# Optimization experiments

Hardware: AMD Instinct MI355X
Metric: run time of the kernel (lower is better)

The kernel has to match this reference:

```python
import jax, jax.numpy as jnp
import numpy as np


def setup_inputs() -> dict:
    key = jax.random.key(0)
    B, E, K = 1024, 1024, 64
    k0, k1, k2, k3, k4, k5 = jax.random.split(key, 6)
    s = 1.0 / np.sqrt(E)  # PyTorch GRU init bound
    c = jax.random.normal(k0, (B, E), dtype=jnp.float32)
    x = jax.random.normal(k1, (B, E, K), dtype=jnp.float32)
    W_ih = jax.random.uniform(k2, (3 * E, E), minval=-s, maxval=s, dtype=jnp.float32)
    W_hh = jax.random.uniform(k3, (3 * E, E), minval=-s, maxval=s, dtype=jnp.float32)
    b_ih = jax.random.uniform(k4, (3 * E,), minval=-s, maxval=s, dtype=jnp.float32)
    b_hh = jax.random.uniform(k5, (3 * E,), minval=-s, maxval=s, dtype=jnp.float32)
    return {"c": c, "x": x, "W_ih": W_ih, "W_hh": W_hh, "b_ih": b_ih, "b_hh": b_hh, "K": K}


def reference(c, x, W_ih, W_hh, b_ih, b_hh, K):
    # c: (B, E) initial hidden state; x: (B, E, T) teacher-forcing sequence.
    # Inputs actually consumed by the GRU: zeros at step 0, then x columns
    # [T-K .. T-2] at steps 1..K-1 (the torch slice at the last step is empty
    # and never used).
    B, E = c.shape
    T = x.shape[2]
    x_t = jnp.transpose(x, (2, 0, 1))  # (T, B, E)
    xs = jnp.concatenate(
        [jnp.zeros((1, B, E), dtype=x.dtype), x_t[T - K : T - 1]], axis=0
    )  # (K, B, E)

    def step(h, xk):
        gi = xk @ W_ih.T + b_ih  # (B, 3E)
        gh = h @ W_hh.T + b_hh   # (B, 3E)
        i_r, i_z, i_n = jnp.split(gi, 3, axis=-1)
        h_r, h_z, h_n = jnp.split(gh, 3, axis=-1)
        r = jax.nn.sigmoid(i_r + h_r)
        z = jax.nn.sigmoid(i_z + h_z)
        n = jnp.tanh(i_n + r * h_n)
        h_new = (1.0 - z) * n + z * h
        return h_new, h_new

    _, ys = jax.lax.scan(step, c, xs)  # ys: (K, B, E)
    y = jnp.transpose(ys, (1, 0, 2))   # (B, K, E) == torch.cat(y_out, dim=1)
    return jnp.transpose(y, (0, 2, 1))  # teacher-forcing transpose -> (B, E, K)
```

## Files before the change

### kernel.cpp

```cpp
#include <hip/hip_runtime.h>
#include <hip/hip_bf16.h>
#include <math.h>

typedef __bf16 bf16x8 __attribute__((ext_vector_type(8)));
typedef float f32x4 __attribute__((ext_vector_type(4)));
typedef unsigned short u16x8 __attribute__((ext_vector_type(8)));

__device__ inline unsigned short f2b(float f) {
  union { float f; unsigned u; } v; v.f = f;
  unsigned u = v.u;
  return (unsigned short)((u + 0x7fffu + ((u >> 16) & 1u)) >> 16);
}
__device__ inline float b2f(unsigned short s) {
  union { unsigned u; float f; } v; v.u = ((unsigned)s) << 16;
  return v.f;
}
__device__ inline float sigm(float x) { return 1.f / (1.f + __expf(-x)); }
__device__ inline float tanh_f(float x) {
  float e = __expf(2.f * x);
  return 1.f - 2.f / (e + 1.f);
}
__device__ inline void gll16(const unsigned short* g, unsigned short* l) {
  __builtin_amdgcn_global_load_lds(
      (const __attribute__((address_space(1))) void*)g,
      (__attribute__((address_space(3))) void*)l, 16, 0, 0);
}
__device__ inline void gll16u(const unsigned short* g, unsigned short* l) {
  __builtin_amdgcn_global_load_lds(
      (const __attribute__((address_space(1))) void*)g,
      (__attribute__((address_space(3))) void*)l, 16, 0, 17);
}
__device__ inline void as64(unsigned short* p, unsigned long long v) {
  __hip_atomic_store((unsigned long long*)p, v, __ATOMIC_RELAXED,
                     __HIP_MEMORY_SCOPE_AGENT);
}

__global__ __launch_bounds__(256) void prep_kernel(
    const float* __restrict__ Wih, const float* __restrict__ Whh,
    const float* __restrict__ c, unsigned short* __restrict__ Wihb,
    unsigned short* __restrict__ Whhb, unsigned short* __restrict__ hbf,
    float* __restrict__ h32, long nW, long nH)
{
  long stride = (long)gridDim.x * blockDim.x;
  long t0 = (long)blockIdx.x * blockDim.x + threadIdx.x;
  for (long i = t0; i < nW; i += stride) {
    Wihb[i] = f2b(Wih[i]);
    Whhb[i] = f2b(Whh[i]);
  }
  for (long i = t0; i < nH; i += stride) {
    float v = c[i];
    h32[i] = v;
    hbf[i] = f2b(v);
  }
}

__global__ __launch_bounds__(256) void reorder_kernel(
    const unsigned short* __restrict__ Wihb, const unsigned short* __restrict__ Whhb,
    const float* __restrict__ bih, const float* __restrict__ bhh,
    unsigned short* __restrict__ Wihp, unsigned short* __restrict__ Whhp,
    float* __restrict__ bihp, float* __restrict__ bhhp, int E)
{
  int N3 = 3 * E;
  long total = (long)N3 * E;
  long stride = (long)gridDim.x * blockDim.x;
  long t0 = (long)blockIdx.x * blockDim.x + threadIdx.x;
  for (long i = t0; i < total; i += stride) {
    int rp = (int)(i / E);
    int col = (int)(i - (long)rp * E);
    int g6 = rp / 192, rem = rp - g6 * 192;
    int g = rem >> 6, elo = rem & 63;
    long src = ((long)g * E + g6 * 64 + elo) * E + col;
    Wihp[i] = Wihb[src];
    Whhp[i] = Whhb[src];
  }
  for (long i = t0; i < N3; i += stride) {
    int rp = (int)i;
    int g6 = rp / 192, rem = rp - g6 * 192;
    int g = rem >> 6, elo = rem & 63;
    bihp[i] = bih[(long)g * E + g6 * 64 + elo];
    bhhp[i] = bhh[(long)g * E + g6 * 64 + elo];
  }
}

__global__ __launch_bounds__(256) void transpose_x(
    const float* __restrict__ x, unsigned short* __restrict__ XS,
    int B, int E, int K)
{
  __shared__ float T[64][65];
  int e0 = blockIdx.x * 64;
  int b = blockIdx.y;
  int t = threadIdx.x;
  const float* xb = x + ((long)b * E + e0) * K;
#pragma unroll
  for (int i = 0; i < 4; ++i) {
    int cidx = i * 256 + t;
    int e = cidx >> 4;
    int f4 = cidx & 15;
    float4 v = *(const float4*)(xb + (long)e * K + f4 * 4);
    T[e][f4 * 4 + 0] = v.x;
    T[e][f4 * 4 + 1] = v.y;
    T[e][f4 * 4 + 2] = v.z;
    T[e][f4 * 4 + 3] = v.w;
  }
  __syncthreads();
#pragma unroll
  for (int i = 0; i < 16; ++i) {
    int cidx = i * 256 + t;
    int k = cidx >> 6;
    int e = cidx & 63;
    if (k < K - 1)
      XS[((long)(k + 1) * B + b) * E + e0 + e] = f2b(T[e][k]);
  }
}

#define BM 128
#define BN 128
#define BKS 64

template<int OUTBF>
__global__ __launch_bounds__(256)
void gemm_bt(const unsigned short* __restrict__ A,
             const unsigned short* __restrict__ Bw,
             const float* __restrict__ bias,
             float* __restrict__ Cf, unsigned short* __restrict__ Cb,
             int M, int N, int K)
{
  __shared__ __align__(16) unsigned short As[BM * BKS];
  __shared__ __align__(16) unsigned short Bs[BN * BKS];

  int nwg = gridDim.x * gridDim.y;
  int wg = blockIdx.y * gridDim.x + blockIdx.x;
  if ((nwg & 7) == 0) { int ch = nwg >> 3; wg = (wg & 7) * ch + (wg >> 3); }
  int tx = wg % gridDim.x;
  int ty = wg / gridDim.x;

  const int tid = threadIdx.x;
  const int lane = tid & 63;
  const int wave = tid >> 6;
  const int wr = wave >> 1, wc = wave & 1;

  f32x4 acc[4][4] = {};

  const long a_base = (long)ty * BM * K;
  const long b_base = (long)tx * BN * K;

  for (int kt = 0; kt < K; kt += BKS) {
    __syncthreads();
#pragma unroll
    for (int i = 0; i < 4; ++i) {
      int c = i * 256 + tid;
      int row = c >> 3, sc = c & 7;
      int gcol8 = sc ^ (row & 7);
      const unsigned short* ga = A + a_base + (long)row * K + kt + gcol8 * 8;
      const unsigned short* gb = Bw + b_base + (long)row * K + kt + gcol8 * 8;
      int cbase = (i * 256 + wave * 64) * 8;
      gll16(ga, &As[cbase]);
      gll16(gb, &Bs[cbase]);
    }
    __syncthreads();
#pragma unroll
    for (int kk = 0; kk < BKS; kk += 32) {
      int kidx = kk + ((lane >> 4) << 3);
      int c8 = kidx >> 3;
      bf16x8 af[4], bfv[4];
#pragma unroll
      for (int m = 0; m < 4; ++m) {
        int row = wr * 64 + m * 16 + (lane & 15);
        af[m] = *(const bf16x8*)&As[row * BKS + ((c8 ^ (row & 7)) << 3)];
      }
#pragma unroll
      for (int n = 0; n < 4; ++n) {
        int col = wc * 64 + n * 16 + (lane & 15);
        bfv[n] = *(const bf16x8*)&Bs[col * BKS + ((c8 ^ (col & 7)) << 3)];
      }
#pragma unroll
      for (int m = 0; m < 4; ++m)
#pragma unroll
        for (int n = 0; n < 4; ++n)
          acc[m][n] = __builtin_amdgcn_mfma_f32_16x16x32_bf16(
              af[m], bfv[n], acc[m][n], 0, 0, 0);
    }
  }

  long crow0 = (long)ty * BM + wr * 64;
  long ccol0 = (long)tx * BN + wc * 64;
#pragma unroll
  for (int m = 0; m < 4; ++m) {
#pragma unroll
    for (int n = 0; n < 4; ++n) {
      long col = ccol0 + n * 16 + (lane & 15);
      float bv = bias[col];
#pragma unroll
      for (int j = 0; j < 4; ++j) {
        long row = crow0 + m * 16 + ((lane >> 4) << 2) + j;
        float v = acc[m][n][j] + bv;
        if (OUTBF) Cb[row * N + col] = f2b(v);
        else       Cf[row * N + col] = v;
      }
    }
  }
}

#define VMW(N) asm volatile("s_waitcnt vmcnt(" #N ")" ::: "memory")

__global__ __launch_bounds__(512, 1)
void gru_rec4(const unsigned short* __restrict__ GI,
              const unsigned short* __restrict__ Whp,
              const float* __restrict__ bhp,
              const unsigned short* __restrict__ h0,
              unsigned short* __restrict__ hbuf0,
              unsigned short* __restrict__ hbuf1,
              unsigned short* __restrict__ Y,
              unsigned int* __restrict__ bar,
              int B, int E, int K, int net)
{
  __shared__ __align__(16) unsigned char smem[156672];
  unsigned short* Ah  = (unsigned short*)smem;
  unsigned short* Bss = (unsigned short*)(smem + 49152);
  unsigned short* GIs = (unsigned short*)(smem + 122880);
  unsigned short* Ys  = (unsigned short*)(smem + 147456);
  float* Red = (float*)smem;

  const int N3 = 3 * E;
  const int e6 = blockIdx.x;
  const int bt = blockIdx.y;
  const int b0 = bt << 6;
  const int ec0 = e6 * 192;
  const int ecol0 = e6 << 6;
  const int tid = threadIdx.x;
  const int lane = tid & 63;
  const int w = tid >> 6;
  const int ew = w >> 1;
  const int kw = w & 1;
  const int q = lane >> 4;
  const int l15 = lane & 15;
  const int el = (ew << 4) + l15;
  const int c8 = (kw << 2) + q;
  const int axo = (c8 ^ (l15 & 7)) << 3;
  const int bxo = (c8 ^ (el & 7)) << 3;

  const int arow = tid >> 3;
  const int ag8 = (tid & 7) ^ (arow & 7);
  const long a_goff = (long)(b0 + arow) * E + ag8 * 8;
  const int a_dst = tid * 8;
  long b_goff[3]; int b_dst[3];
#pragma unroll
  for (int i = 0; i < 3; ++i) {
    int c = i * 512 + tid;
    int row = c >> 3;
    int g8 = (c & 7) ^ (row & 7);
    b_goff[i] = (long)(ec0 + row) * E + g8 * 8;
    b_dst[i] = c * 8;
  }
  long gi_off[3]; int gi_dst[3];
#pragma unroll
  for (int i = 0; i < 3; ++i) {
    int c = i * 512 + tid;
    int row = c / 24, cc = c - row * 24;
    gi_off[i] = (long)(b0 + row) * N3 + ec0 + cc * 8;
    gi_dst[i] = c * 8;
  }

  const float bh0 = bhp[ec0 + el];
  const float bh1 = bhp[ec0 + 64 + el];
  const float bh2 = bhp[ec0 + 128 + el];

  if (kw == 0) {
#pragma unroll
    for (int m = 0; m < 4; ++m)
#pragma unroll
      for (int j = 0; j < 4; ++j) {
        int row = m * 16 + q * 4 + j;
        Ys[row * 72 + el] = h0[(long)(b0 + row) * E + ecol0 + el];
      }
  }
  __syncthreads();

  for (int k = 0; k < K; ++k) {
    const unsigned short* hprev = (k & 1) ? hbuf1 : hbuf0;
    unsigned short* hnext = (k & 1) ? hbuf0 : hbuf1;
    const unsigned short* GIk = GI + (long)k * B * N3;

#pragma unroll
    for (int i = 0; i < 3; ++i) gll16(GIk + gi_off[i], GIs + gi_dst[i]);
#pragma unroll
    for (int t = 0; t < 5; ++t)
      gll16u(hprev + a_goff + t * 64, Ah + t * 4096 + a_dst);
#pragma unroll
    for (int t = 0; t < 2; ++t)
#pragma unroll
      for (int i = 0; i < 3; ++i)
        gll16(Whp + b_goff[i] + t * 64, Bss + t * 12288 + b_dst[i]);

    f32x4 acc[4][3];
#pragma unroll
    for (int m = 0; m < 4; ++m)
#pragma unroll
      for (int g = 0; g < 3; ++g)
        acc[m][g] = (f32x4){0.f, 0.f, 0.f, 0.f};

#pragma unroll
    for (int kt = 0; kt < 16; ++kt) {
      if (kt == 0)       VMW(3);
      else if (kt == 1)  VMW(4);
      else if (kt <= 11) VMW(5);
      else if (kt == 12) VMW(4);
      else if (kt == 15) VMW(0);
      else               VMW(3);
      asm volatile("s_waitcnt lgkmcnt(0)" ::: "memory");
      __builtin_amdgcn_s_barrier();
      asm volatile("" ::: "memory");

      if (kt + 2 < 16) {
#pragma unroll
        for (int i = 0; i < 3; ++i)
          gll16(Whp + b_goff[i] + (kt + 2) * 64,
                Bss + ((kt + 2) % 3) * 12288 + b_dst[i]);
      }
      if (kt + 5 < 16)
        gll16u(hprev + a_goff + (kt + 5) * 64,
               Ah + ((kt + 5) % 6) * 4096 + a_dst);

      const unsigned short* Ab = Ah + (kt % 6) * 4096;
      const unsigned short* Bb = Bss + (kt % 3) * 12288;
      bf16x8 af[4], bfg[3];
#pragma unroll
      for (int m = 0; m < 4; ++m)
        af[m] = *(const bf16x8*)&Ab[(m * 16 + l15) * 64 + axo];
#pragma unroll
      for (int g = 0; g < 3; ++g)
        bfg[g] = *(const bf16x8*)&Bb[(g * 64 + el) * 64 + bxo];

      __builtin_amdgcn_s_setprio(1);
#pragma unroll
      for (int g = 0; g < 3; ++g)
#pragma unroll
        for (int m = 0; m < 4; ++m)
          acc[m][g] = __builtin_amdgcn_mfma_f32_16x16x32_bf16(
              af[m], bfg[g], acc[m][g], 0, 0, 0);
      __builtin_amdgcn_s_setprio(0);
    }

    __syncthreads();
    float* rp = &Red[((ew << 6) + lane) * 49];
    if (kw == 1) {
#pragma unroll
      for (int m = 0; m < 4; ++m)
#pragma unroll
        for (int g = 0; g < 3; ++g)
#pragma unroll
          for (int cc = 0; cc < 4; ++cc)
            rp[(m * 3 + g) * 4 + cc] = acc[m][g][cc];
    }
    __syncthreads();
    if (kw == 0) {
#pragma unroll
      for (int m = 0; m < 4; ++m) {
#pragma unroll
        for (int j = 0; j < 4; ++j) {
          int row = m * 16 + q * 4 + j;
          float ghr = acc[m][0][j] + rp[(m * 3 + 0) * 4 + j];
          float ghz = acc[m][1][j] + rp[(m * 3 + 1) * 4 + j];
          float ghn = acc[m][2][j] + rp[(m * 3 + 2) * 4 + j];
          float gr = b2f(GIs[row * 192 + el]);
          float gz = b2f(GIs[row * 192 + 64 + el]);
          float gn = b2f(GIs[row * 192 + 128 + el]);
          float hu = b2f(Ys[row * 72 + el]);
          float r = sigm(gr + ghr + bh0);
          float z = sigm(gz + ghz + bh1);
          float n = tanh_f(gn + r * (ghn + bh2));
          float hv = (1.f - z) * n + z * hu;
          Ys[row * 72 + el] = f2b(hv);
        }
      }
    }
    __syncthreads();
    {
      int row = tid >> 3, cc = tid & 7;
      u16x8 v = *(const u16x8*)&Ys[row * 72 + cc * 8];
      unsigned* pv = (unsigned*)&v;
      unsigned long long s0 = ((unsigned long long)pv[1] << 32) | pv[0];
      unsigned long long s1 = ((unsigned long long)pv[3] << 32) | pv[2];
      unsigned short* hp = hnext + (long)(b0 + row) * E + ecol0 + cc * 8;
      as64(hp, s0);
      as64(hp + 4, s1);
      *(u16x8*)(Y + ((long)k * B + b0 + row) * E + ecol0 + cc * 8) = v;
    }
    if (k + 1 < K) {
      __syncthreads();
      if (tid == 0) {
        __hip_atomic_fetch_add(&bar[bt * 64], 1u, __ATOMIC_RELAXED,
                               __HIP_MEMORY_SCOPE_AGENT);
        unsigned target = (unsigned)(k + 1) * (unsigned)net;
        while (__hip_atomic_load(&bar[bt * 64], __ATOMIC_RELAXED,
                                 __HIP_MEMORY_SCOPE_AGENT) < target)
          __builtin_amdgcn_s_sleep(1);
      }
      __syncthreads();
    }
  }
}

template<int YMODE>
__global__ __launch_bounds__(256)
void gru_pointwise(const unsigned short* __restrict__ GIk,
                   const float* __restrict__ gh,
                   float* __restrict__ h, unsigned short* __restrict__ hbf,
                   unsigned short* __restrict__ Yb,
                   float* __restrict__ out, int k, int B, int E, int K)
{
  long i4 = ((long)blockIdx.x * blockDim.x + threadIdx.x) * 4;
  if (i4 >= (long)B * E) return;
  long b = i4 / E;
  long e = i4 - b * E;
  long g0 = b * 3 * E + e;
  ushort4 ir = *(const ushort4*)(GIk + g0);
  ushort4 iz = *(const ushort4*)(GIk + g0 + E);
  ushort4 in4 = *(const ushort4*)(GIk + g0 + 2 * E);
  float4 hr = *(const float4*)(gh + g0);
  float4 hz = *(const float4*)(gh + g0 + E);
  float4 hn = *(const float4*)(gh + g0 + 2 * E);
  float4 hv = *(const float4*)(h + i4);

  float irf[4] = { b2f(ir.x), b2f(ir.y), b2f(ir.z), b2f(ir.w) };
  float izf[4] = { b2f(iz.x), b2f(iz.y), b2f(iz.z), b2f(iz.w) };
  float inf_[4] = { b2f(in4.x), b2f(in4.y), b2f(in4.z), b2f(in4.w) };
  float hrf[4] = { hr.x, hr.y, hr.z, hr.w };
  float hzf[4] = { hz.x, hz.y, hz.z, hz.w };
  float hnf[4] = { hn.x, hn.y, hn.z, hn.w };
  float hvf[4] = { hv.x, hv.y, hv.z, hv.w };
  float hnew[4];
#pragma unroll
  for (int j = 0; j < 4; ++j) {
    float r = sigm(irf[j] + hrf[j]);
    float z = sigm(izf[j] + hzf[j]);
    float n = tanh_f(inf_[j] + r * hnf[j]);
    hnew[j] = (1.f - z) * n + z * hvf[j];
  }
  *(float4*)(h + i4) = make_float4(hnew[0], hnew[1], hnew[2], hnew[3]);
  ushort4 hb = make_ushort4(f2b(hnew[0]), f2b(hnew[1]), f2b(hnew[2]), f2b(hnew[3]));
  *(ushort4*)(hbf + i4) = hb;
  if (YMODE == 1) {
    *(ushort4*)(Yb + ((long)k * B + b) * E + e) = hb;
  } else {
    float* o = out + (b * E + e) * K + k;
    o[0] = hnew[0]; o[K] = hnew[1]; o[2 * K] = hnew[2]; o[3 * K] = hnew[3];
  }
}

__global__ __launch_bounds__(256)
void transpose_y(const unsigned short* __restrict__ Yv, float* __restrict__ out,
                 int B, int E, int K)
{
  __shared__ float T[64][65];
  int e0 = blockIdx.x * 64;
  int b = blockIdx.y;
  int t = threadIdx.x;
#pragma unroll
  for (int i = 0; i < 4; ++i) {
    int c = i * 256 + t;
    int k = c >> 4, f4 = c & 15;
    long off = ((long)k * B + b) * E + e0 + f4 * 4;
    ushort4 v = *(const ushort4*)(Yv + off);
    T[k][f4 * 4 + 0] = b2f(v.x); T[k][f4 * 4 + 1] = b2f(v.y);
    T[k][f4 * 4 + 2] = b2f(v.z); T[k][f4 * 4 + 3] = b2f(v.w);
  }
  __syncthreads();
#pragma unroll
  for (int i = 0; i < 4; ++i) {
    int c = i * 256 + t;
    int e = c >> 4, f4k = c & 15;
    float4 w;
    w.x = T[f4k * 4 + 0][e];
    w.y = T[f4k * 4 + 1][e];
    w.z = T[f4k * 4 + 2][e];
    w.w = T[f4k * 4 + 3][e];
    *(float4*)(out + ((long)b * E + e0 + e) * K + f4k * 4) = w;
  }
}

extern "C" void kernel_launch(void* const* d_in, const int* in_sizes, int n_in,
                              void* d_out, int out_size, void* d_ws, size_t ws_size,
                              hipStream_t stream)
{
  const float* c   = (const float*)d_in[0];
  const float* x   = (const float*)d_in[1];
  const float* Wih = (const float*)d_in[2];
  const float* Whh = (const float*)d_in[3];
  const float* bih = (const float*)d_in[4];
  const float* bhh = (const float*)d_in[5];
  float* out = (float*)d_out;

  long BE = in_sizes[0];
  int E = (int)(sqrtf((float)(in_sizes[2] / 3)) + 0.5f);
  int B = (int)(BE / E);
  int K = (int)(in_sizes[1] / BE);
  int N3 = 3 * E;
  long M_GI = (long)K * B;

  char* w = (char*)d_ws;
  size_t used = 0;
  auto alloc = [&](size_t bytes) -> char* {
    char* p = w + used;
    used += (bytes + 255) & ~(size_t)255;
    return p;
  };
  unsigned short* Wihb  = (unsigned short*)alloc((size_t)N3 * E * 2);
  unsigned short* Whhb  = (unsigned short*)alloc((size_t)N3 * E * 2);
  unsigned short* hb0   = (unsigned short*)alloc((size_t)B * E * 2);
  float* h32            = (float*)alloc((size_t)B * E * 4);
  float* gh             = (float*)alloc((size_t)B * N3 * 4);
  unsigned short* GIstep= (unsigned short*)alloc((size_t)B * N3 * 2);
  unsigned short* XS    = (unsigned short*)alloc((size_t)K * B * E * 2);

  size_t rem = (ws_size > used) ? ws_size - used : 0;
  size_t szW   = (((size_t)N3 * E * 2) + 255) & ~(size_t)255;
  size_t szB3  = (((size_t)N3 * 4) + 255) & ~(size_t)255;
  size_t szHb1 = (((size_t)B * E * 2) + 255) & ~(size_t)255;
  size_t szGI  = (((size_t)K * B * N3 * 2) + 255) & ~(size_t)255;
  size_t szY   = (((size_t)K * B * E * 2) + 255) & ~(size_t)255;
  int nbt = B / 64, net = E / 64;
  size_t szBar = ((size_t)nbt * 64 * 4 + 255) & ~(size_t)255;

  bool canFused = (B == 1024) && (E == 1024) &&
                  (rem >= 2 * szW + 2 * szB3 + szHb1 + szGI + szY + szBar);

  long nW = (long)N3 * E;
  prep_kernel<<<dim3(2048), dim3(256), 0, stream>>>(Wih, Whh, c, Wihb, Whhb,
                                                    hb0, h32, nW, BE);
  hipMemsetAsync(XS, 0, (size_t)B * E * 2, stream);
  transpose_x<<<dim3(E / 64, B), dim3(256), 0, stream>>>(x, XS, B, E, K);

  if (canFused) {
    unsigned short* Wihp = (unsigned short*)alloc(szW);
    unsigned short* Whhp = (unsigned short*)alloc(szW);
    float* bihp          = (float*)alloc(szB3);
    float* bhhp          = (float*)alloc(szB3);
    unsigned short* hb1  = (unsigned short*)alloc(szHb1);
    unsigned short* GI   = (unsigned short*)alloc(szGI);
    unsigned short* Yb   = (unsigned short*)alloc(szY);
    unsigned int*   bar  = (unsigned int*)alloc(szBar);

    reorder_kernel<<<dim3(2048), dim3(256), 0, stream>>>(
        Wihb, Whhb, bih, bhh, Wihp, Whhp, bihp, bhhp, E);

    gemm_bt<1><<<dim3(N3 / BN, (int)(M_GI / BM)), dim3(256), 0, stream>>>(
        XS, Wihp, bihp, nullptr, GI, (int)M_GI, N3, E);
    hipMemsetAsync(bar, 0, szBar, stream);

    const unsigned short* GIc = GI;
    const unsigned short* Whhc = Whhp;
    const float* bhhc = bhhp;
    const unsigned short* h0c = hb0;
    void* args[] = { (void*)&GIc, (void*)&Whhc, (void*)&bhhc, (void*)&h0c,
                     (void*)&hb0, (void*)&hb1, (void*)&Yb,
                     (void*)&bar, (void*)&B, (void*)&E, (void*)&K, (void*)&net };
    hipError_t ce = hipLaunchCooperativeKernel(
        (const void*)gru_rec4, dim3(net, nbt), dim3(512), args, 0, stream);
    if (ce != hipSuccess) {
      (void)hipGetLastError();
      gru_rec4<<<dim3(net, nbt), dim3(512), 0, stream>>>(
          GIc, Whhc, bhhc, h0c, hb0, hb1, Yb, bar, B, E, K, net);
    }
    transpose_y<<<dim3(E / 64, B), dim3(256), 0, stream>>>(Yb, out, B, E, K);
    return;
  }

  int haveY = rem >= szY;
  unsigned short* Yb = haveY ? (unsigned short*)alloc(szY) : nullptr;
  int pgrid = (int)((BE / 4 + 255) / 256);
  for (int k = 0; k < K; ++k) {
    gemm_bt<1><<<dim3(N3 / BN, B / BM), dim3(256), 0, stream>>>(
        XS + (size_t)k * B * E, Wihb, bih, nullptr, GIstep, B, N3, E);
    gemm_bt<0><<<dim3(N3 / BN, B / BM), dim3(256), 0, stream>>>(
        hb0, Whhb, bhh, gh, nullptr, B, N3, E);
    if (haveY)
      gru_pointwise<1><<<dim3(pgrid), dim3(256), 0, stream>>>(
          GIstep, gh, h32, hb0, Yb, out, k, B, E, K);
    else
      gru_pointwise<2><<<dim3(pgrid), dim3(256), 0, stream>>>(
          GIstep, gh, h32, hb0, nullptr, out, k, B, E, K);
  }
  if (haveY)
    transpose_y<<<dim3(E / 64, B), dim3(256), 0, stream>>>(Yb, out, B, E, K);
}
```

Baseline: 1.625 ms.

## Prefetch next-step GI and first weight tiles before the inter-block barrier

```diff
diff --git a/kernel.cpp b/kernel.cpp
--- a/kernel.cpp
+++ b/kernel.cpp
@@ -202,9 +202,10 @@
 }
 
 #define VMW(N) asm volatile("s_waitcnt vmcnt(" #N ")" ::: "memory")
+#define LGKM0  asm volatile("s_waitcnt lgkmcnt(0)" ::: "memory")
 
 __global__ __launch_bounds__(512, 1)
-void gru_rec4(const unsigned short* __restrict__ GI,
+void gru_rec5(const unsigned short* __restrict__ GI,
               const unsigned short* __restrict__ Whp,
               const float* __restrict__ bhp,
               const unsigned short* __restrict__ h0,
@@ -276,21 +277,20 @@
   }
   __syncthreads();
 
+#pragma unroll
+  for (int i = 0; i < 3; ++i) gll16u(GI + gi_off[i], GIs + gi_dst[i]);
+#pragma unroll
+  for (int i = 0; i < 3; ++i) gll16(Whp + b_goff[i], Bss + b_dst[i]);
+#pragma unroll
+  for (int i = 0; i < 3; ++i) gll16(Whp + b_goff[i] + 64, Bss + 12288 + b_dst[i]);
+
   for (int k = 0; k < K; ++k) {
     const unsigned short* hprev = (k & 1) ? hbuf1 : hbuf0;
     unsigned short* hnext = (k & 1) ? hbuf0 : hbuf1;
-    const unsigned short* GIk = GI + (long)k * B * N3;
-
-#pragma unroll
-    for (int i = 0; i < 3; ++i) gll16(GIk + gi_off[i], GIs + gi_dst[i]);
+
 #pragma unroll
     for (int t = 0; t < 5; ++t)
       gll16u(hprev + a_goff + t * 64, Ah + t * 4096 + a_dst);
-#pragma unroll
-    for (int t = 0; t < 2; ++t)
-#pragma unroll
-      for (int i = 0; i < 3; ++i)
-        gll16(Whp + b_goff[i] + t * 64, Bss + t * 12288 + b_dst[i]);
 
     f32x4 acc[4][3];
 #pragma unroll
@@ -301,28 +301,27 @@
 
 #pragma unroll
     for (int kt = 0; kt < 16; ++kt) {
-      if (kt == 0)       VMW(3);
-      else if (kt == 1)  VMW(4);
+      if (kt == 0)       VMW(4);
+      else if (kt == 1)  VMW(7);
       else if (kt <= 11) VMW(5);
       else if (kt == 12) VMW(4);
       else if (kt == 15) VMW(0);
       else               VMW(3);
-      asm volatile("s_waitcnt lgkmcnt(0)" ::: "memory");
+      LGKM0;
       __builtin_amdgcn_s_barrier();
       asm volatile("" ::: "memory");
 
-      if (kt + 2 < 16) {
+      if (kt <= 13) {
+        int sl = (k + kt + 2) % 3;
 #pragma unroll
         for (int i = 0; i < 3; ++i)
-          gll16(Whp + b_goff[i] + (kt + 2) * 64,
-                Bss + ((kt + 2) % 3) * 12288 + b_dst[i]);
+          gll16(Whp + b_goff[i] + (kt + 2) * 64, Bss + sl * 12288 + b_dst[i]);
       }
-      if (kt + 5 < 16)
-        gll16u(hprev + a_goff + (kt + 5) * 64,
-               Ah + ((kt + 5) % 6) * 4096 + a_dst);
+      if (kt <= 10)
+        gll16u(hprev + a_goff + (kt + 5) * 64, Ah + ((kt + 5) % 6) * 4096 + a_dst);
 
       const unsigned short* Ab = Ah + (kt % 6) * 4096;
-      const unsigned short* Bb = Bss + (kt % 3) * 12288;
+      const unsigned short* Bb = Bss + ((k + kt) % 3) * 12288;
       bf16x8 af[4], bfg[3];
 #pragma unroll
       for (int m = 0; m < 4; ++m)
@@ -341,7 +340,9 @@
       __builtin_amdgcn_s_setprio(0);
     }
 
-    __syncthreads();
+    LGKM0;
+    __builtin_amdgcn_s_barrier();
+    asm volatile("" ::: "memory");
     float* rp = &Red[((ew << 6) + lane) * 49];
     if (kw == 1) {
 #pragma unroll
@@ -352,7 +353,9 @@
           for (int cc = 0; cc < 4; ++cc)
             rp[(m * 3 + g) * 4 + cc] = acc[m][g][cc];
     }
-    __syncthreads();
+    LGKM0;
+    __builtin_amdgcn_s_barrier();
+    asm volatile("" ::: "memory");
     if (kw == 0) {
 #pragma unroll
       for (int m = 0; m < 4; ++m) {
@@ -374,7 +377,9 @@
         }
       }
     }
-    __syncthreads();
+    LGKM0;
+    __builtin_amdgcn_s_barrier();
+    asm volatile("" ::: "memory");
     {
       int row = tid >> 3, cc = tid & 7;
       u16x8 v = *(const u16x8*)&Ys[row * 72 + cc * 8];
@@ -384,10 +389,24 @@
       unsigned short* hp = hnext + (long)(b0 + row) * E + ecol0 + cc * 8;
       as64(hp, s0);
       as64(hp + 4, s1);
-      *(u16x8*)(Y + ((long)k * B + b0 + row) * E + ecol0 + cc * 8) = v;
+      unsigned short* yp = Y + ((long)k * B + b0 + row) * E + ecol0 + cc * 8;
+      as64(yp, s0);
+      as64(yp + 4, s1);
     }
     if (k + 1 < K) {
-      __syncthreads();
+      const unsigned short* GIn = GI + (long)(k + 1) * B * N3;
+#pragma unroll
+      for (int i = 0; i < 3; ++i) gll16u(GIn + gi_off[i], GIs + gi_dst[i]);
+      int sl0 = (k + 1) % 3, sl1 = (k + 2) % 3;
+#pragma unroll
+      for (int i = 0; i < 3; ++i)
+        gll16(Whp + b_goff[i], Bss + sl0 * 12288 + b_dst[i]);
+#pragma unroll
+      for (int i = 0; i < 3; ++i)
+        gll16(Whp + b_goff[i] + 64, Bss + sl1 * 12288 + b_dst[i]);
+      VMW(9);
+      __builtin_amdgcn_s_barrier();
+      asm volatile("" ::: "memory");
       if (tid == 0) {
         __hip_atomic_fetch_add(&bar[bt * 64], 1u, __ATOMIC_RELAXED,
                                __HIP_MEMORY_SCOPE_AGENT);
@@ -396,7 +415,8 @@
                                  __HIP_MEMORY_SCOPE_AGENT) < target)
           __builtin_amdgcn_s_sleep(1);
       }
-      __syncthreads();
+      __builtin_amdgcn_s_barrier();
+      asm volatile("" ::: "memory");
     }
   }
 }
@@ -556,10 +576,10 @@
                      (void*)&hb0, (void*)&hb1, (void*)&Yb,
                      (void*)&bar, (void*)&B, (void*)&E, (void*)&K, (void*)&net };
     hipError_t ce = hipLaunchCooperativeKernel(
-        (const void*)gru_rec4, dim3(net, nbt), dim3(512), args, 0, stream);
+        (const void*)gru_rec5, dim3(net, nbt), dim3(512), args, 0, stream);
     if (ce != hipSuccess) {
       (void)hipGetLastError();
-      gru_rec4<<<dim3(net, nbt), dim3(512), 0, stream>>>(
+      gru_rec5<<<dim3(net, nbt), dim3(512), 0, stream>>>(
           GIc, Whhc, bhhc, h0c, hb0, hb1, Yb, bar, B, E, K, net);
     }
     transpose_y<<<dim3(E / 64, B), dim3(256), 0, stream>>>(Yb, out, B, E, K);
```

New measurement: 1.772 ms. 9.0% more time.

## Replace input-projection GEMM with 128x256 tile, 512-thread, triple-buffered kernel

Applied to the files above, without the earlier changes.

```diff
diff --git a/kernel.cpp b/kernel.cpp
--- a/kernel.cpp
+++ b/kernel.cpp
@@ -5,6 +5,10 @@
 typedef __bf16 bf16x8 __attribute__((ext_vector_type(8)));
 typedef float f32x4 __attribute__((ext_vector_type(4)));
 typedef unsigned short u16x8 __attribute__((ext_vector_type(8)));
+
+#define VMW(N) asm volatile("s_waitcnt vmcnt(" #N ")" ::: "memory")
+#define LGKM0  asm volatile("s_waitcnt lgkmcnt(0)" ::: "memory")
+#define CFENCE asm volatile("" ::: "memory")
 
 __device__ inline unsigned short f2b(float f) {
   union { float f; unsigned u; } v; v.f = f;
@@ -113,6 +117,164 @@
   }
 }
 
+__global__ __launch_bounds__(512, 1)
+void gemm256(const unsigned short* __restrict__ A,
+             const unsigned short* __restrict__ Bw,
+             const float* __restrict__ bias,
+             unsigned short* __restrict__ Cb,
+             int M, int N, int K)
+{
+  __shared__ __align__(16) unsigned short sm[3 * 24576];
+
+  int nwg = gridDim.x * gridDim.y;
+  int wg = blockIdx.y * gridDim.x + blockIdx.x;
+  if ((nwg & 7) == 0) { int ch = nwg >> 3; wg = (wg & 7) * ch + (wg >> 3); }
+  int tx = wg % gridDim.x;
+  int ty = wg / gridDim.x;
+
+  const int tid = threadIdx.x;
+  const int lane = tid & 63;
+  const int wave = tid >> 6;
+  const int wm = wave >> 2;
+  const int wn = wave & 3;
+  const int q = lane >> 4;
+  const int l15 = lane & 15;
+
+  const long a_base = (long)ty * 128 * K;
+  const long b_base = (long)tx * 256 * K;
+
+  long a_src[2]; int a_dst[2];
+#pragma unroll
+  for (int i = 0; i < 2; ++i) {
+    int c = i * 512 + tid;
+    int row = c >> 3;
+    int g8 = (c & 7) ^ (row & 7);
+    a_src[i] = a_base + (long)row * K + g8 * 8;
+    a_dst[i] = c * 8;
+  }
+  long b_src[4]; int b_dst[4];
+#pragma unroll
+  for (int i = 0; i < 4; ++i) {
+    int c = i * 512 + tid;
+    int row = c >> 3;
+    int g8 = (c & 7) ^ (row & 7);
+    b_src[i] = b_base + (long)row * K + g8 * 8;
+    b_dst[i] = c * 8;
+  }
+
+  int a_ro[4], b_ro[4];
+#pragma unroll
+  for (int mi = 0; mi < 4; ++mi) {
+    int lr = wm * 64 + mi * 16 + l15;
+    a_ro[mi] = lr * 64;
+  }
+#pragma unroll
+  for (int ni = 0; ni < 4; ++ni) {
+    int col = wn * 64 + ni * 16 + l15;
+    b_ro[ni] = col * 64;
+  }
+
+  f32x4 acc[4][4] = {};
+
+  const int NT = K >> 6;
+#pragma unroll
+  for (int t = 0; t < 2; ++t) {
+    unsigned short* As = sm + t * 24576;
+    unsigned short* Bs = As + 8192;
+#pragma unroll
+    for (int i = 0; i < 2; ++i) gll16(A + a_src[i] + t * 64, As + a_dst[i]);
+#pragma unroll
+    for (int i = 0; i < 4; ++i) gll16(Bw + b_src[i] + t * 64, Bs + b_dst[i]);
+  }
+
+  for (int kt = 0; kt < NT; ++kt) {
+    if (kt >= NT - 2) VMW(0); else VMW(6);
+    __builtin_amdgcn_s_barrier();
+    CFENCE;
+    const unsigned short* As = sm + (kt % 3) * 24576;
+    const unsigned short* Bs = As + 8192;
+    unsigned short* As2 = sm + ((kt + 2) % 3) * 24576;
+    unsigned short* Bs2 = As2 + 8192;
+    const bool st = (kt + 2 < NT);
+    const int ko = (kt + 2) * 64;
+
+    if (st) {
+      gll16(A + a_src[0] + ko, As2 + a_dst[0]);
+      gll16(A + a_src[1] + ko, As2 + a_dst[1]);
+      gll16(Bw + b_src[0] + ko, Bs2 + b_dst[0]);
+    }
+    {
+      const int c8 = q;
+      bf16x8 af[4], bf_[4];
+#pragma unroll
+      for (int mi = 0; mi < 4; ++mi) {
+        int lr = wm * 64 + mi * 16 + l15;
+        af[mi] = *(const bf16x8*)&As[a_ro[mi] + ((c8 ^ (lr & 7)) << 3)];
+      }
+#pragma unroll
+      for (int ni = 0; ni < 4; ++ni) {
+        int col = wn * 64 + ni * 16 + l15;
+        bf_[ni] = *(const bf16x8*)&Bs[b_ro[ni] + ((c8 ^ (col & 7)) << 3)];
+      }
+      __builtin_amdgcn_s_setprio(1);
+#pragma unroll
+      for (int mi = 0; mi < 4; ++mi)
+#pragma unroll
+        for (int ni = 0; ni < 4; ++ni)
+          acc[mi][ni] = __builtin_amdgcn_mfma_f32_16x16x32_bf16(
+              af[mi], bf_[ni], acc[mi][ni], 0, 0, 0);
+      __builtin_amdgcn_s_setprio(0);
+    }
+    LGKM0;
+    __builtin_amdgcn_s_barrier();
+    CFENCE;
+    if (st) {
+      gll16(Bw + b_src[1] + ko, Bs2 + b_dst[1]);
+      gll16(Bw + b_src[2] + ko, Bs2 + b_dst[2]);
+      gll16(Bw + b_src[3] + ko, Bs2 + b_dst[3]);
+    }
+    {
+      const int c8 = 4 + q;
+      bf16x8 af[4], bf_[4];
+#pragma unroll
+      for (int mi = 0; mi < 4; ++mi) {
+        int lr = wm * 64 + mi * 16 + l15;
+        af[mi] = *(const bf16x8*)&As[a_ro[mi] + ((c8 ^ (lr & 7)) << 3)];
+      }
+#pragma unroll
+      for (int ni = 0; ni < 4; ++ni) {
+        int col = wn * 64 + ni * 16 + l15;
+        bf_[ni] = *(const bf16x8*)&Bs[b_ro[ni] + ((c8 ^ (col & 7)) << 3)];
+      }
+      __builtin_amdgcn_s_setprio(1);
+#pragma unroll
+      for (int mi = 0; mi < 4; ++mi)
+#pragma unroll
+        for (int ni = 0; ni < 4; ++ni)
+          acc[mi][ni] = __builtin_amdgcn_mfma_f32_16x16x32_bf16(
+              af[mi], bf_[ni], acc[mi][ni], 0, 0, 0);
+      __builtin_amdgcn_s_setprio(0);
+    }
+    LGKM0;
+  }
+
+  long crow0 = (long)ty * 128 + wm * 64;
+  long ccol0 = (long)tx * 256 + wn * 64;
+#pragma unroll
+  for (int mi = 0; mi < 4; ++mi) {
+#pragma unroll
+    for (int ni = 0; ni < 4; ++ni) {
+      long col = ccol0 + ni * 16 + l15;
+      float bv = bias[col];
+#pragma unroll
+      for (int j = 0; j < 4; ++j) {
+        long row = crow0 + mi * 16 + (q << 2) + j;
+        Cb[row * N + col] = f2b(acc[mi][ni][j] + bv);
+      }
+    }
+  }
+}
+
 #define BM 128
 #define BN 128
 #define BKS 64
@@ -200,8 +362,6 @@
     }
   }
 }
-
-#define VMW(N) asm volatile("s_waitcnt vmcnt(" #N ")" ::: "memory")
 
 __global__ __launch_bounds__(512, 1)
 void gru_rec4(const unsigned short* __restrict__ GI,
@@ -307,9 +467,9 @@
       else if (kt == 12) VMW(4);
       else if (kt == 15) VMW(0);
       else               VMW(3);
-      asm volatile("s_waitcnt lgkmcnt(0)" ::: "memory");
+      LGKM0;
       __builtin_amdgcn_s_barrier();
-      asm volatile("" ::: "memory");
+      CFENCE;
 
       if (kt + 2 < 16) {
 #pragma unroll
@@ -544,8 +704,8 @@
     reorder_kernel<<<dim3(2048), dim3(256), 0, stream>>>(
         Wihb, Whhb, bih, bhh, Wihp, Whhp, bihp, bhhp, E);
 
-    gemm_bt<1><<<dim3(N3 / BN, (int)(M_GI / BM)), dim3(256), 0, stream>>>(
-        XS, Wihp, bihp, nullptr, GI, (int)M_GI, N3, E);
+    gemm256<<<dim3(N3 / 256, (int)(M_GI / 128)), dim3(512), 0, stream>>>(
+        XS, Wihp, bihp, GI, (int)M_GI, N3, E);
     hipMemsetAsync(bar, 0, szBar, stream);
 
     const unsigned short* GIc = GI;
```

Result: faster. 1.480 ms (-8.9%).

## Fuse input-projection GEMM into persistent GRU recurrence kernel

Applied to the files above, without the earlier changes.

```diff
diff --git a/kernel.cpp b/kernel.cpp
--- a/kernel.cpp
+++ b/kernel.cpp
@@ -5,6 +5,10 @@
 typedef __bf16 bf16x8 __attribute__((ext_vector_type(8)));
 typedef float f32x4 __attribute__((ext_vector_type(4)));
 typedef unsigned short u16x8 __attribute__((ext_vector_type(8)));
+
+#define VMW(N) asm volatile("s_waitcnt vmcnt(" #N ")" ::: "memory")
+#define LGKM0  asm volatile("s_waitcnt lgkmcnt(0)" ::: "memory")
+#define CFENCE asm volatile("" ::: "memory")
 
 __device__ inline unsigned short f2b(float f) {
   union { float f; unsigned u; } v; v.f = f;
@@ -54,11 +58,13 @@
   }
 }
 
-__global__ __launch_bounds__(256) void reorder_kernel(
-    const unsigned short* __restrict__ Wihb, const unsigned short* __restrict__ Whhb,
-    const float* __restrict__ bih, const float* __restrict__ bhh,
+__global__ __launch_bounds__(256) void prep2_kernel(
+    const float* __restrict__ Wih, const float* __restrict__ Whh,
+    const float* __restrict__ c, const float* __restrict__ bih,
+    const float* __restrict__ bhh,
     unsigned short* __restrict__ Wihp, unsigned short* __restrict__ Whhp,
-    float* __restrict__ bihp, float* __restrict__ bhhp, int E)
+    float* __restrict__ bihp, float* __restrict__ bhhp,
+    unsigned short* __restrict__ hb0, int E, long nH)
 {
   int N3 = 3 * E;
   long total = (long)N3 * E;
@@ -70,8 +76,8 @@
     int g6 = rp / 192, rem = rp - g6 * 192;
     int g = rem >> 6, elo = rem & 63;
     long src = ((long)g * E + g6 * 64 + elo) * E + col;
-    Wihp[i] = Wihb[src];
-    Whhp[i] = Whhb[src];
+    Wihp[i] = f2b(Wih[src]);
+    Whhp[i] = f2b(Whh[src]);
   }
   for (long i = t0; i < N3; i += stride) {
     int rp = (int)i;
@@ -80,6 +86,8 @@
     bihp[i] = bih[(long)g * E + g6 * 64 + elo];
     bhhp[i] = bhh[(long)g * E + g6 * 64 + elo];
   }
+  for (long i = t0; i < nH; i += stride)
+    hb0[i] = f2b(c[i]);
 }
 
 __global__ __launch_bounds__(256) void transpose_x(
@@ -201,27 +209,30 @@
   }
 }
 
-#define VMW(N) asm volatile("s_waitcnt vmcnt(" #N ")" ::: "memory")
-
 __global__ __launch_bounds__(512, 1)
-void gru_rec4(const unsigned short* __restrict__ GI,
-              const unsigned short* __restrict__ Whp,
-              const float* __restrict__ bhp,
-              const unsigned short* __restrict__ h0,
-              unsigned short* __restrict__ hbuf0,
-              unsigned short* __restrict__ hbuf1,
-              unsigned short* __restrict__ Y,
-              unsigned int* __restrict__ bar,
-              int B, int E, int K, int net)
+void gru_rec10(const unsigned short* __restrict__ XS,
+               const unsigned short* __restrict__ Wihp,
+               const unsigned short* __restrict__ Whhp,
+               const float* __restrict__ bihp,
+               const float* __restrict__ bhhp,
+               const unsigned short* __restrict__ h0,
+               unsigned short* __restrict__ hbuf0,
+               unsigned short* __restrict__ hbuf1,
+               unsigned short* __restrict__ Y,
+               unsigned int* __restrict__ bar,
+               int B, int E, int K, int net)
 {
   __shared__ __align__(16) unsigned char smem[156672];
-  unsigned short* Ah  = (unsigned short*)smem;
-  unsigned short* Bss = (unsigned short*)(smem + 49152);
-  unsigned short* GIs = (unsigned short*)(smem + 122880);
+  unsigned short* Bih = (unsigned short*)smem;
+  unsigned short* Bhh = (unsigned short*)(smem + 49152);
+  unsigned short* Axs = (unsigned short*)(smem + 98304);
+  unsigned short* Ah  = (unsigned short*)(smem + 114688);
   unsigned short* Ys  = (unsigned short*)(smem + 147456);
-  float* Red = (float*)smem;
+  float* Red1 = (float*)smem;
+  float* Red2 = (float*)(smem + 51200);
 
   const int N3 = 3 * E;
+  const long BE = (long)B * E;
   const int e6 = blockIdx.x;
   const int bt = blockIdx.y;
   const int b0 = bt << 6;
@@ -246,24 +257,27 @@
   long b_goff[3]; int b_dst[3];
 #pragma unroll
   for (int i = 0; i < 3; ++i) {
-    int c = i * 512 + tid;
-    int row = c >> 3;
-    int g8 = (c & 7) ^ (row & 7);
+    int cc = i * 512 + tid;
+    int row = cc >> 3;
+    int g8 = (cc & 7) ^ (row & 7);
     b_goff[i] = (long)(ec0 + row) * E + g8 * 8;
-    b_dst[i] = c * 8;
-  }
-  long gi_off[3]; int gi_dst[3];
-#pragma unroll
-  for (int i = 0; i < 3; ++i) {
-    int c = i * 512 + tid;
-    int row = c / 24, cc = c - row * 24;
-    gi_off[i] = (long)(b0 + row) * N3 + ec0 + cc * 8;
-    gi_dst[i] = c * 8;
-  }
-
-  const float bh0 = bhp[ec0 + el];
-  const float bh1 = bhp[ec0 + 64 + el];
-  const float bh2 = bhp[ec0 + 128 + el];
+    b_dst[i] = cc * 8;
+  }
+
+  const float bhv0 = bhhp[ec0 + el];
+  const float bhv1 = bhhp[ec0 + 64 + el];
+  const float bhv2 = bhhp[ec0 + 128 + el];
+  const float biv0 = bihp[ec0 + el];
+  const float biv1 = bihp[ec0 + 64 + el];
+  const float biv2 = bihp[ec0 + 128 + el];
+
+  unsigned short gireg[3][16];
+#pragma unroll
+  for (int i = 0; i < 16; ++i) {
+    gireg[0][i] = f2b(biv0);
+    gireg[1][i] = f2b(biv1);
+    gireg[2][i] = f2b(biv2);
+  }
 
   if (kw == 0) {
 #pragma unroll
@@ -279,78 +293,105 @@
   for (int k = 0; k < K; ++k) {
     const unsigned short* hprev = (k & 1) ? hbuf1 : hbuf0;
     unsigned short* hnext = (k & 1) ? hbuf0 : hbuf1;
-    const unsigned short* GIk = GI + (long)k * B * N3;
-
-#pragma unroll
-    for (int i = 0; i < 3; ++i) gll16(GIk + gi_off[i], GIs + gi_dst[i]);
-#pragma unroll
-    for (int t = 0; t < 5; ++t)
+    int xsk = (k + 1 < K) ? (k + 1) : (K - 1);
+    const unsigned short* XSk = XS + (long)xsk * BE;
+
+#pragma unroll
+    for (int i = 0; i < 3; ++i) gll16(Wihp + b_goff[i], Bih + b_dst[i]);
+#pragma unroll
+    for (int i = 0; i < 3; ++i) gll16(Whhp + b_goff[i], Bhh + b_dst[i]);
+    gll16(XSk + a_goff, Axs + a_dst);
+#pragma unroll
+    for (int t = 0; t < 3; ++t)
       gll16u(hprev + a_goff + t * 64, Ah + t * 4096 + a_dst);
-#pragma unroll
-    for (int t = 0; t < 2; ++t)
-#pragma unroll
-      for (int i = 0; i < 3; ++i)
-        gll16(Whp + b_goff[i] + t * 64, Bss + t * 12288 + b_dst[i]);
-
-    f32x4 acc[4][3];
+
+    f32x4 acc_gh[4][3], acc_gi[4][3];
 #pragma unroll
     for (int m = 0; m < 4; ++m)
 #pragma unroll
-      for (int g = 0; g < 3; ++g)
-        acc[m][g] = (f32x4){0.f, 0.f, 0.f, 0.f};
-
-#pragma unroll
-    for (int kt = 0; kt < 16; ++kt) {
-      if (kt == 0)       VMW(3);
-      else if (kt == 1)  VMW(4);
-      else if (kt <= 11) VMW(5);
-      else if (kt == 12) VMW(4);
-      else if (kt == 15) VMW(0);
-      else               VMW(3);
-      asm volatile("s_waitcnt lgkmcnt(0)" ::: "memory");
+      for (int g = 0; g < 3; ++g) {
+        acc_gh[m][g] = (f32x4){0.f, 0.f, 0.f, 0.f};
+        acc_gi[m][g] = (f32x4){0.f, 0.f, 0.f, 0.f};
+      }
+
+#pragma unroll
+    for (int c = 0; c < 16; ++c) {
+      if (c == 0)       VMW(2);
+      else if (c <= 13) VMW(1);
+      else              VMW(0);
+      LGKM0;
       __builtin_amdgcn_s_barrier();
-      asm volatile("" ::: "memory");
-
-      if (kt + 2 < 16) {
+      CFENCE;
+
+      if (c + 1 < 16) {
 #pragma unroll
         for (int i = 0; i < 3; ++i)
-          gll16(Whp + b_goff[i] + (kt + 2) * 64,
-                Bss + ((kt + 2) % 3) * 12288 + b_dst[i]);
-      }
-      if (kt + 5 < 16)
-        gll16u(hprev + a_goff + (kt + 5) * 64,
-               Ah + ((kt + 5) % 6) * 4096 + a_dst);
-
-      const unsigned short* Ab = Ah + (kt % 6) * 4096;
-      const unsigned short* Bb = Bss + (kt % 3) * 12288;
-      bf16x8 af[4], bfg[3];
+          gll16(Wihp + b_goff[i] + (c + 1) * 64,
+                Bih + ((c + 1) & 1) * 12288 + b_dst[i]);
+#pragma unroll
+        for (int i = 0; i < 3; ++i)
+          gll16(Whhp + b_goff[i] + (c + 1) * 64,
+                Bhh + ((c + 1) & 1) * 12288 + b_dst[i]);
+        gll16(XSk + a_goff + (c + 1) * 64, Axs + ((c + 1) & 1) * 4096 + a_dst);
+      }
+      if (c + 3 < 16)
+        gll16u(hprev + a_goff + (c + 3) * 64,
+               Ah + ((c + 3) & 3) * 4096 + a_dst);
+
+      {
+        const unsigned short* Ax = Axs + (c & 1) * 4096;
+        const unsigned short* Bi = Bih + (c & 1) * 12288;
+        bf16x8 af[4], bfg[3];
+#pragma unroll
+        for (int m = 0; m < 4; ++m)
+          af[m] = *(const bf16x8*)&Ax[(m * 16 + l15) * 64 + axo];
+#pragma unroll
+        for (int g = 0; g < 3; ++g)
+          bfg[g] = *(const bf16x8*)&Bi[(g * 64 + el) * 64 + bxo];
+        __builtin_amdgcn_s_setprio(1);
+#pragma unroll
+        for (int g = 0; g < 3; ++g)
+#pragma unroll
+          for (int m = 0; m < 4; ++m)
+            acc_gi[m][g] = __builtin_amdgcn_mfma_f32_16x16x32_bf16(
+                af[m], bfg[g], acc_gi[m][g], 0, 0, 0);
+        __builtin_amdgcn_s_setprio(0);
+      }
+      {
+        const unsigned short* Ax = Ah + (c & 3) * 4096;
+        const unsigned short* Bh = Bhh + (c & 1) * 12288;
+        bf16x8 af[4], bfg[3];
+#pragma unroll
+        for (int m = 0; m < 4; ++m)
+          af[m] = *(const bf16x8*)&Ax[(m * 16 + l15) * 64 + axo];
+#pragma unroll
+        for (int g = 0; g < 3; ++g)
+          bfg[g] = *(const bf16x8*)&Bh[(g * 64 + el) * 64 + bxo];
+        __builtin_amdgcn_s_setprio(1);
+#pragma unroll
+        for (int g = 0; g < 3; ++g)
+#pragma unroll
+          for (int m = 0; m < 4; ++m)
+            acc_gh[m][g] = __builtin_amdgcn_mfma_f32_16x16x32_bf16(
+                af[m], bfg[g], acc_gh[m][g], 0, 0, 0);
+        __builtin_amdgcn_s_setprio(0);
+      }
+    }
+
+    LGKM0;
+    __syncthreads();
+    float* rp1 = &Red1[((ew << 6) + lane) * 49];
+    float* rp2 = &Red2[((ew << 6) + lane) * 49];
+    if (kw == 1) {
 #pragma unroll
       for (int m = 0; m < 4; ++m)
-        af[m] = *(const bf16x8*)&Ab[(m * 16 + l15) * 64 + axo];
-#pragma unroll
-      for (int g = 0; g < 3; ++g)
-        bfg[g] = *(const bf16x8*)&Bb[(g * 64 + el) * 64 + bxo];
-
-      __builtin_amdgcn_s_setprio(1);
-#pragma unroll
-      for (int g = 0; g < 3; ++g)
-#pragma unroll
-        for (int m = 0; m < 4; ++m)
-          acc[m][g] = __builtin_amdgcn_mfma_f32_16x16x32_bf16(
-              af[m], bfg[g], acc[m][g], 0, 0, 0);
-      __builtin_amdgcn_s_setprio(0);
-    }
-
-    __syncthreads();
-    float* rp = &Red[((ew << 6) + lane) * 49];
-    if (kw == 1) {
-#pragma unroll
-      for (int m = 0; m < 4; ++m)
 #pragma unroll
         for (int g = 0; g < 3; ++g)
 #pragma unroll
-          for (int cc = 0; cc < 4; ++cc)
-            rp[(m * 3 + g) * 4 + cc] = acc[m][g][cc];
+          for (int cc = 0; cc < 4; ++cc) {
+            rp1[(m * 3 + g) * 4 + cc] = acc_gh[m][g][cc];
+            rp2[(m * 3 + g) * 4 + cc] = acc_gi[m][g][cc];
+          }
     }
     __syncthreads();
     if (kw == 0) {
@@ -359,19 +400,32 @@
 #pragma unroll
         for (int j = 0; j < 4; ++j) {
           int row = m * 16 + q * 4 + j;
-          float ghr = acc[m][0][j] + rp[(m * 3 + 0) * 4 + j];
-          float ghz = acc[m][1][j] + rp[(m * 3 + 1) * 4 + j];
-          float ghn = acc[m][2][j] + rp[(m * 3 + 2) * 4 + j];
-          float gr = b2f(GIs[row * 192 + el]);
-          float gz = b2f(GIs[row * 192 + 64 + el]);
-          float gn = b2f(GIs[row * 192 + 128 + el]);
+          float ghr = acc_gh[m][0][j] + rp1[(m * 3 + 0) * 4 + j];
+          float ghz = acc_gh[m][1][j] + rp1[(m * 3 + 1) * 4 + j];
+          float ghn = acc_gh[m][2][j] + rp1[(m * 3 + 2) * 4 + j];
+          float gr = b2f(gireg[0][m * 4 + j]);
+          float gz = b2f(gireg[1][m * 4 + j]);
+          float gn = b2f(gireg[2][m * 4 + j]);
           float hu = b2f(Ys[row * 72 + el]);
-          float r = sigm(gr + ghr + bh0);
-          float z = sigm(gz + ghz + bh1);
-          float n = tanh_f(gn + r * (ghn + bh2));
+          float r = sigm(gr + ghr + bhv0);
+          float z = sigm(gz + ghz + bhv1);
+          float n = tanh_f(gn + r * (ghn + bhv2));
           float hv = (1.f - z) * n + z * hu;
           Ys[row * 72 + el] = f2b(hv);
         }
+      }
+      if (k + 1 < K) {
+#pragma unroll
+        for (int m = 0; m < 4; ++m)
+#pragma unroll
+          for (int j = 0; j < 4; ++j) {
+            gireg[0][m * 4 + j] =
+                f2b(acc_gi[m][0][j] + rp2[(m * 3 + 0) * 4 + j] + biv0);
+            gireg[1][m * 4 + j] =
+                f2b(acc_gi[m][1][j] + rp2[(m * 3 + 1) * 4 + j] + biv1);
+            gireg[2][m * 4 + j] =
+                f2b(acc_gi[m][2][j] + rp2[(m * 3 + 2) * 4 + j] + biv2);
+          }
       }
     }
     __syncthreads();
@@ -496,7 +550,6 @@
   int B = (int)(BE / E);
   int K = (int)(in_sizes[1] / BE);
   int N3 = 3 * E;
-  long M_GI = (long)K * B;
 
   char* w = (char*)d_ws;
   size_t used = 0;
@@ -505,25 +558,65 @@
     used += (bytes + 255) & ~(size_t)255;
     return p;
   };
-  unsigned short* Wihb  = (unsigned short*)alloc((size_t)N3 * E * 2);
-  unsigned short* Whhb  = (unsigned short*)alloc((size_t)N3 * E * 2);
-  unsigned short* hb0   = (unsigned short*)alloc((size_t)B * E * 2);
+  unsigned short* XS = (unsigned short*)alloc((size_t)K * B * E * 2);
+
+  size_t szW   = (((size_t)N3 * E * 2) + 255) & ~(size_t)255;
+  size_t szB3  = (((size_t)N3 * 4) + 255) & ~(size_t)255;
+  size_t szHb  = (((size_t)B * E * 2) + 255) & ~(size_t)255;
+  size_t szY   = (((size_t)K * B * E * 2) + 255) & ~(size_t)255;
+  int nbt = B / 64, net = E / 64;
+  size_t szBar = ((size_t)nbt * 64 * 4 + 255) & ~(size_t)255;
+
+  size_t needFused = 2 * szW + 2 * szB3 + 2 * szHb + szY + szBar;
+  bool canFused = (B == 1024) && (E == 1024) && (K == 64) &&
+                  (ws_size > used) && ((ws_size - used) >= needFused);
+
+  if (canFused) {
+    unsigned short* Wihp = (unsigned short*)alloc(szW);
+    unsigned short* Whhp = (unsigned short*)alloc(szW);
+    float* bihp          = (float*)alloc(szB3);
+    float* bhhp          = (float*)alloc(szB3);
+    unsigned short* hb0  = (unsigned short*)alloc(szHb);
+    unsigned short* hb1  = (unsigned short*)alloc(szHb);
+    unsigned short* Yb   = (unsigned short*)alloc(szY);
+    unsigned int*   bar  = (unsigned int*)alloc(szBar);
+
+    prep2_kernel<<<dim3(2048), dim3(256), 0, stream>>>(
+        Wih, Whh, c, bih, bhh, Wihp, Whhp, bihp, bhhp, hb0, E, BE);
+    hipMemsetAsync(XS, 0, (size_t)B * E * 2, stream);
+    transpose_x<<<dim3(E / 64, B), dim3(256), 0, stream>>>(x, XS, B, E, K);
+    hipMemsetAsync(bar, 0, szBar, stream);
+
+    const unsigned short* XSc = XS;
+    const unsigned short* Wihc = Wihp;
+    const unsigned short* Whhc = Whhp;
+    const float* bihc = bihp;
+    const float* bhhc = bhhp;
+    const unsigned short* h0c = hb0;
+    void* args[] = { (void*)&XSc, (void*)&Wihc, (void*)&Whhc,
+                     (void*)&bihc, (void*)&bhhc, (void*)&h0c,
+                     (void*)&hb0, (void*)&hb1, (void*)&Yb,
+                     (void*)&bar, (void*)&B, (void*)&E, (void*)&K, (void*)&net };
+    hipError_t ce = hipLaunchCooperativeKernel(
+        (const void*)gru_rec10, dim3(net, nbt), dim3(512), args, 0, stream);
+    if (ce != hipSuccess) {
+      (void)hipGetLastError();
+      gru_rec10<<<dim3(net, nbt), dim3(512), 0, stream>>>(
+          XSc, Wihc, Whhc, bihc, bhhc, h0c, hb0, hb1, Yb, bar, B, E, K, net);
+    }
+    transpose_y<<<dim3(E / 64, B), dim3(256), 0, stream>>>(Yb, out, B, E, K);
+    return;
+  }
+
+  unsigned short* Wihb  = (unsigned short*)alloc(szW);
+  unsigned short* Whhb  = (unsigned short*)alloc(szW);
+  unsigned short* hb0   = (unsigned short*)alloc(szHb);
   float* h32            = (float*)alloc((size_t)B * E * 4);
   float* gh             = (float*)alloc((size_t)B * N3 * 4);
   unsigned short* GIstep= (unsigned short*)alloc((size_t)B * N3 * 2);
-  unsigned short* XS    = (unsigned short*)alloc((size_t)K * B * E * 2);
-
   size_t rem = (ws_size > used) ? ws_size - used : 0;
-  size_t szW   = (((size_t)N3 * E * 2) + 255) & ~(size_t)255;
-  size_t szB3  = (((size_t)N3 * 4) + 255) & ~(size_t)255;
-  size_t szHb1 = (((size_t)B * E * 2) + 255) & ~(size_t)255;
-  size_t szGI  = (((size_t)K * B * N3 * 2) + 255) & ~(size_t)255;
-  size_t szY   = (((size_t)K * B * E * 2) + 255) & ~(size_t)255;
-  int nbt = B / 64, net = E / 64;
-  size_t szBar = ((size_t)nbt * 64 * 4 + 255) & ~(size_t)255;
-
-  bool canFused = (B == 1024) && (E == 1024) &&
-                  (rem >= 2 * szW + 2 * szB3 + szHb1 + szGI + szY + szBar);
+  int haveY = rem >= szY;
+  unsigned short* Yb = haveY ? (unsigned short*)alloc(szY) : nullptr;
 
   long nW = (long)N3 * E;
   prep_kernel<<<dim3(2048), dim3(256), 0, stream>>>(Wih, Whh, c, Wihb, Whhb,
@@ -531,43 +624,6 @@
   hipMemsetAsync(XS, 0, (size_t)B * E * 2, stream);
   transpose_x<<<dim3(E / 64, B), dim3(256), 0, stream>>>(x, XS, B, E, K);
 
-  if (canFused) {
-    unsigned short* Wihp = (unsigned short*)alloc(szW);
-    unsigned short* Whhp = (unsigned short*)alloc(szW);
-    float* bihp          = (float*)alloc(szB3);
-    float* bhhp          = (float*)alloc(szB3);
-    unsigned short* hb1  = (unsigned short*)alloc(szHb1);
-    unsigned short* GI   = (unsigned short*)alloc(szGI);
-    unsigned short* Yb   = (unsigned short*)alloc(szY);
-    unsigned int*   bar  = (unsigned int*)alloc(szBar);
-
-    reorder_kernel<<<dim3(2048), dim3(256), 0, stream>>>(
-        Wihb, Whhb, bih, bhh, Wihp, Whhp, bihp, bhhp, E);
-
-    gemm_bt<1><<<dim3(N3 / BN, (int)(M_GI / BM)), dim3(256), 0, stream>>>(
-        XS, Wihp, bihp, nullptr, GI, (int)M_GI, N3, E);
-    hipMemsetAsync(bar, 0, szBar, stream);
-
-    const unsigned short* GIc = GI;
-    const unsigned short* Whhc = Whhp;
-    const float* bhhc = bhhp;
-    const unsigned short* h0c = hb0;
-    void* args[] = { (void*)&GIc, (void*)&Whhc, (void*)&bhhc, (void*)&h0c,
-                     (void*)&hb0, (void*)&hb1, (void*)&Yb,
-                     (void*)&bar, (void*)&B, (void*)&E, (void*)&K, (void*)&net };
-    hipError_t ce = hipLaunchCooperativeKernel(
-        (const void*)gru_rec4, dim3(net, nbt), dim3(512), args, 0, stream);
-    if (ce != hipSuccess) {
-      (void)hipGetLastError();
-      gru_rec4<<<dim3(net, nbt), dim3(512), 0, stream>>>(
-          GIc, Whhc, bhhc, h0c, hb0, hb1, Yb, bar, B, E, K, net);
-    }
-    transpose_y<<<dim3(E / 64, B), dim3(256), 0, stream>>>(Yb, out, B, E, K);
-    return;
-  }
-
-  int haveY = rem >= szY;
-  unsigned short* Yb = haveY ? (unsigned short*)alloc(szY) : nullptr;
   int pgrid = (int)((BE / 4 + 255) / 256);
   for (int k = 0; k < K; ++k) {
     gemm_bt<1><<<dim3(N3 / BN, B / BM), dim3(256), 0, stream>>>(
```

After: 2.885 ms. 1.78x slower.
